# Optimization experiments

Hardware: AMD Instinct MI355X
Metric: run time of the kernel (lower is better)

Reference implementation:

```python
import jax, jax.numpy as jnp
import numpy as np

N_NODES = 50000
N_EDGES = 600000
N_RELS = 16
N_GRAPHS = 128
IN_DIM = 128
REL_LAYERS = [128, 256, 128]
HIDDEN = [128, 256, 128]
N_CLASSES = 8


def setup_inputs() -> dict:
    key = jax.random.key(0)
    ks = jax.random.split(key, 24)
    inp = {}
    inp["h"] = jax.random.normal(ks[0], (N_NODES, IN_DIM), dtype=jnp.float32)
    inp["src"] = jax.random.randint(ks[1], (N_EDGES,), 0, N_NODES)
    inp["dst"] = jax.random.randint(ks[2], (N_EDGES,), 0, N_NODES)
    inp["rel_types"] = jax.random.randint(ks[3], (N_EDGES,), 0, N_RELS)
    inp["graph_ids"] = jnp.sort(jax.random.randint(ks[4], (N_NODES,), 0, N_GRAPHS))
    # RelGraphConv params per layer: W_rel [R,din,dout], W_loop [din,dout], b [dout]
    prev = IN_DIM
    ki = 5
    for i, d in enumerate(REL_LAYERS):
        inp[f"W_rel{i}"] = jax.random.normal(ks[ki], (N_RELS, prev, d), dtype=jnp.float32) * 0.05
        inp[f"W_loop{i}"] = jax.random.normal(ks[ki + 1], (prev, d), dtype=jnp.float32) * 0.05
        inp[f"b{i}"] = jnp.zeros((d,), dtype=jnp.float32)
        prev = d
        ki += 2
    for i, d in enumerate(HIDDEN):
        inp[f"Wh{i}"] = jax.random.normal(ks[ki], (prev, d), dtype=jnp.float32) * 0.05
        inp[f"bh{i}"] = jnp.zeros((d,), dtype=jnp.float32)
        prev = d
        ki += 1
    inp["Wc"] = jax.random.normal(ks[ki], (prev, N_CLASSES), dtype=jnp.float32) * 0.05
    inp["bc"] = jnp.zeros((N_CLASSES,), dtype=jnp.float32)
    return inp


def _rel_graph_conv(h, src, dst, rel, W_rel, W_loop, b):
    # transform every node under every relation: [R, N, dout]
    t = jnp.einsum("nd,rde->rne", h, W_rel)
    msgs = t[rel, src]  # [E, dout] gather per edge
    agg = jax.ops.segment_sum(msgs, dst, num_segments=h.shape[0])
    return jax.nn.relu(agg + h @ W_loop + b)  # self-loop + bias (DGL defaults)


def _forward(h, src, dst, rel_types, graph_ids,
             W_rel0, W_loop0, b0, W_rel1, W_loop1, b1, W_rel2, W_loop2, b2,
             Wh0, bh0, Wh1, bh1, Wh2, bh2, Wc, bc):
    h = h.astype(jnp.float32)
    for Wr, Wl, b in ((W_rel0, W_loop0, b0), (W_rel1, W_loop1, b1), (W_rel2, W_loop2, b2)):
        h = _rel_graph_conv(h, src, dst, rel_types, Wr, Wl, b)
    # dgl.mean_nodes: per-graph mean pooling
    sums = jax.ops.segment_sum(h, graph_ids, num_segments=N_GRAPHS)
    cnts = jax.ops.segment_sum(jnp.ones((h.shape[0],), h.dtype), graph_ids, num_segments=N_GRAPHS)
    hg = sums / jnp.maximum(cnts, 1.0)[:, None]
    for W, b in ((Wh0, bh0), (Wh1, bh1), (Wh2, bh2)):
        hg = jax.nn.relu(hg @ W + b)
    return jax.nn.softmax(hg @ Wc + bc, axis=1)


def reference(h, src, dst, rel_types, graph_ids,
              W_rel0, W_loop0, b0, W_rel1, W_loop1, b1, W_rel2, W_loop2, b2,
              Wh0, bh0, Wh1, bh1, Wh2, bh2, Wc, bc):
    return _forward(h, src, dst, rel_types, graph_ids,
                    W_rel0, W_loop0, b0, W_rel1, W_loop1, b1, W_rel2, W_loop2, b2,
                    Wh0, bh0, Wh1, bh1, Wh2, bh2, Wc, bc)
```

## Files before the change

kernel.cpp:

```cpp
#include <hip/hip_runtime.h>
#include <stdint.h>

#define NN 50000
#define NE 600000
#define NR 16
#define NG 128
#define TS 128
#define SCAN_B 512
#define NB_SCAN ((NN + SCAN_B - 1) / SCAN_B)
#define MAXB 1024

typedef short bf16x8 __attribute__((ext_vector_type(8)));
typedef float f32x4 __attribute__((ext_vector_type(4)));

static __device__ __forceinline__ unsigned short f2bf(float x) {
    unsigned int b = __float_as_uint(x);
    b += 0x7FFFu + ((b >> 16) & 1u);
    return (unsigned short)(b >> 16);
}
static __device__ __forceinline__ float bf2f(unsigned short u) {
    return __uint_as_float(((unsigned int)u) << 16);
}


__global__ void k_hist(const int* __restrict__ rel, const int* __restrict__ dst,
                       const int* __restrict__ src,
                       int* __restrict__ bcnt, int* __restrict__ ncnt,
                       int npc, int nps, int SB, int B) {
    __shared__ int lh[MAXB];
    for (int i = threadIdx.x; i < B; i += 256) lh[i] = 0;
    __syncthreads();
    for (int e = blockIdx.x * blockDim.x + threadIdx.x; e < NE; e += gridDim.x * blockDim.x) {
        int d = dst[e];
        int key = (d / npc) * SB + (src[e] / nps) * NR + rel[e];
        atomicAdd(&lh[key], 1);
        atomicAdd(&ncnt[d], 1);
    }
    __syncthreads();
    for (int i = threadIdx.x; i < B; i += 256) atomicAdd(&bcnt[i], lh[i]);
}

__global__ void k_scan1(const int* __restrict__ ncnt, int* __restrict__ bsum) {
    __shared__ int s[SCAN_B];
    int i = blockIdx.x * SCAN_B + threadIdx.x;
    s[threadIdx.x] = (i < NN) ? ncnt[i] : 0;
    __syncthreads();
    for (int off = SCAN_B / 2; off > 0; off >>= 1) {
        if (threadIdx.x < off) s[threadIdx.x] += s[threadIdx.x + off];
        __syncthreads();
    }
    if (threadIdx.x == 0) bsum[blockIdx.x] = s[0];
}

__global__ void k_scan2(const int* __restrict__ bsum, int* __restrict__ bpref, int* __restrict__ rowptr) {
    if (threadIdx.x == 0 && blockIdx.x == 0) {
        int run = 0;
        for (int b = 0; b < NB_SCAN; ++b) { bpref[b] = run; run += bsum[b]; }
        rowptr[NN] = run;
    }
}

__global__ void k_scan3(const int* __restrict__ ncnt, const int* __restrict__ bpref,
                        int* __restrict__ rowptr) {
    __shared__ int s[SCAN_B];
    int i = blockIdx.x * SCAN_B + threadIdx.x;
    int val = (i < NN) ? ncnt[i] : 0;
    s[threadIdx.x] = val;
    __syncthreads();
    for (int off = 1; off < SCAN_B; off <<= 1) {
        int x = (threadIdx.x >= off) ? s[threadIdx.x - off] : 0;
        __syncthreads();
        s[threadIdx.x] += x;
        __syncthreads();
    }
    if (i < NN) rowptr[i] = bpref[blockIdx.x] + s[threadIdx.x] - val;
}

__global__ __launch_bounds__(1024)
void k_scan_buckets(const int* __restrict__ bcnt, int B, int npc, int SB,
                    const int* __restrict__ rowptr,
                    int* __restrict__ boff, int* __restrict__ tstart,
                    int4* __restrict__ tilemap) {
    __shared__ int s1[MAXB], s2[MAXB];
    __shared__ int e_ex[MAXB + 1], t_ex[MAXB + 1];
    int tid = threadIdx.x;
    int v1 = (tid < B) ? bcnt[tid] : 0;
    int v2 = (v1 + TS - 1) / TS;
    s1[tid] = v1; s2[tid] = v2;
    __syncthreads();
    for (int off = 1; off < MAXB; off <<= 1) {
        int a1 = (tid >= off) ? s1[tid - off] : 0;
        int a2 = (tid >= off) ? s2[tid - off] : 0;
        __syncthreads();
        s1[tid] += a1; s2[tid] += a2;
        __syncthreads();
    }
    if (tid < B) {
        e_ex[tid] = s1[tid] - v1;
        t_ex[tid] = s2[tid] - v2;
        boff[tid] = e_ex[tid];
        tstart[tid] = t_ex[tid];
        if (tid == B - 1) {
            e_ex[B] = s1[tid]; t_ex[B] = s2[tid];
            boff[B] = s1[tid]; tstart[B] = s2[tid];
        }
    }
    __syncthreads();
    int T = t_ex[B];
    for (int t = tid; t < T; t += 1024) {
        int lo = 0, hi = B - 1;
        while (lo < hi) {
            int mid = (lo + hi + 1) >> 1;
            if (t_ex[mid] <= t) lo = mid; else hi = mid - 1;
        }
        int b = lo;
        int tt = t - t_ex[b];
        int v1b = e_ex[b + 1] - e_ex[b];
        int rem = v1b - tt * TS;
        int cnt = rem < TS ? rem : TS;
        int chunk = b / SB;
        int nstart = chunk * npc; if (nstart > NN) nstart = NN;
        tilemap[t] = make_int4(b & (NR - 1), e_ex[b] + tt * TS, cnt, rowptr[nstart]);
    }
}

__global__ void k_scatter(const int* __restrict__ rel, const int* __restrict__ dst,
                          const int* __restrict__ src,
                          const int* __restrict__ boff, int* __restrict__ cursor,
                          const int* __restrict__ rowptr, int* __restrict__ ncur,
                          int* __restrict__ srcs, int* __restrict__ dpos,
                          int npc, int nps, int SB, int B) {
    __shared__ int lh[MAXB];
    const int CH = 4096;
    int e0 = blockIdx.x * CH;
    for (int i = threadIdx.x; i < B; i += 256) lh[i] = 0;
    __syncthreads();
    for (int i = threadIdx.x; i < CH; i += 256) {
        int e = e0 + i;
        if (e < NE) atomicAdd(&lh[(dst[e] / npc) * SB + (src[e] / nps) * NR + rel[e]], 1);
    }
    __syncthreads();
    for (int i = threadIdx.x; i < B; i += 256) {
        int c = lh[i];
        lh[i] = (c > 0) ? atomicAdd(&cursor[i], c) : 0;
    }
    __syncthreads();
    for (int i = threadIdx.x; i < CH; i += 256) {
        int e = e0 + i;
        if (e < NE) {
            int d = dst[e];
            int s = src[e];
            int b = (d / npc) * SB + (s / nps) * NR + rel[e];
            int p = boff[b] + atomicAdd(&lh[b], 1);
            int pd = rowptr[d] + atomicAdd(&ncur[d], 1);
            srcs[p] = s;
            dpos[p] = pd;
        }
    }
}


__global__ void k_hconv(const float* __restrict__ h, unsigned short* __restrict__ hb, int n4) {
    int i = blockIdx.x * 256 + threadIdx.x;
    if (i < n4) {
        float4 v = reinterpret_cast<const float4*>(h)[i];
        ushort4 o = { f2bf(v.x), f2bf(v.y), f2bf(v.z), f2bf(v.w) };
        reinterpret_cast<ushort4*>(hb)[i] = o;
    }
}

__global__ void k_wconv_all(const float* Wr0, const float* Wr1, const float* Wr2,
                            const float* Wl0, const float* Wl1, const float* Wl2,
                            unsigned short* Wt0, unsigned short* Wt1, unsigned short* Wt2,
                            unsigned short* Wlt0, unsigned short* Wlt1, unsigned short* Wlt2) {
    const float* W; unsigned short* O; int R, Kd, Nd;
    switch (blockIdx.y) {
        case 0:  W = Wr0; O = Wt0;  R = NR; Kd = 128; Nd = 128; break;
        case 1:  W = Wr1; O = Wt1;  R = NR; Kd = 128; Nd = 256; break;
        case 2:  W = Wr2; O = Wt2;  R = NR; Kd = 256; Nd = 128; break;
        case 3:  W = Wl0; O = Wlt0; R = 1;  Kd = 128; Nd = 128; break;
        case 4:  W = Wl1; O = Wlt1; R = 1;  Kd = 128; Nd = 256; break;
        default: W = Wl2; O = Wlt2; R = 1;  Kd = 256; Nd = 128; break;
    }
    int total = R * Kd * Nd;
    for (int i = blockIdx.x * 256 + threadIdx.x; i < total; i += gridDim.x * 256) {
        int r = i / (Kd * Nd);
        int rem = i - r * Kd * Nd;
        int k = rem / Nd;
        int n = rem - k * Nd;
        O[((size_t)r * Nd + n) * Kd + k] = f2bf(W[i]);
    }
}


template<int K>
__global__ __launch_bounds__(256, 4)
void k_dense_mfma(const unsigned short* __restrict__ hb,
                  const unsigned short* __restrict__ Wlt,
                  const float* __restrict__ bias,
                  float* __restrict__ outbuf, int ldn) {
    __shared__ __align__(16) unsigned short As[128][72];
    __shared__ __align__(16) unsigned short Bs[128][72];
    const int tid = threadIdx.x;
    const int row0 = blockIdx.x * 128;
    const int colbase = blockIdx.y * 128;
    const int lane = tid & 63, w = tid >> 6;
    const int quad = lane >> 4, col = lane & 15;
    const int srow = tid >> 3, sk = (tid & 7) * 8;

    f32x4 acc[8][2];
#pragma unroll
    for (int i = 0; i < 8; ++i) { acc[i][0] = 0.f; acc[i][1] = 0.f; }

    for (int k0 = 0; k0 < K; k0 += 64) {
        __syncthreads();
#pragma unroll
        for (int pp = 0; pp < 4; ++pp) {
            int rw = pp * 32 + srow;
            int ar = row0 + rw; if (ar >= NN) ar = NN - 1;
            *reinterpret_cast<uint4*>(&As[rw][sk]) =
                *reinterpret_cast<const uint4*>(hb + (size_t)ar * K + k0 + sk);
            *reinterpret_cast<uint4*>(&Bs[rw][sk]) =
                *reinterpret_cast<const uint4*>(Wlt + (size_t)(colbase + rw) * K + k0 + sk);
        }
        __syncthreads();
#pragma unroll
        for (int s = 0; s < 2; ++s) {
            bf16x8 bf0 = *reinterpret_cast<const bf16x8*>(&Bs[w * 32 + col][s * 32 + quad * 8]);
            bf16x8 bf1 = *reinterpret_cast<const bf16x8*>(&Bs[w * 32 + 16 + col][s * 32 + quad * 8]);
#pragma unroll
            for (int rt = 0; rt < 8; ++rt) {
                bf16x8 af = *reinterpret_cast<const bf16x8*>(&As[rt * 16 + col][s * 32 + quad * 8]);
                acc[rt][0] = __builtin_amdgcn_mfma_f32_16x16x32_bf16(af, bf0, acc[rt][0], 0, 0, 0);
                acc[rt][1] = __builtin_amdgcn_mfma_f32_16x16x32_bf16(af, bf1, acc[rt][1], 0, 0, 0);
            }
        }
    }
    float bv0 = bias[colbase + w * 32 + col];
    float bv1 = bias[colbase + w * 32 + 16 + col];
#pragma unroll
    for (int rt = 0; rt < 8; ++rt) {
#pragma unroll
        for (int reg = 0; reg < 4; ++reg) {
            int r = row0 + rt * 16 + quad * 4 + reg;
            if (r < NN) {
                float* dp = outbuf + (size_t)r * ldn + colbase + w * 32;
                dp[col] = acc[rt][0][reg] + bv0;
                dp[16 + col] = acc[rt][1][reg] + bv1;
            }
        }
    }
}


template<int K>
__global__ __launch_bounds__(256, 4)
void k_edge_mfma(const unsigned short* __restrict__ hb,
                 const unsigned short* __restrict__ Wt,
                 int ldn, int colbase,
                 const int* __restrict__ srcs, const int* __restrict__ dpos,
                 const int4* __restrict__ tilemap, const int* __restrict__ tstart,
                 int chunkBase, int SB,
                 unsigned short* __restrict__ msg, int capRows) {
    const int tb0 = tstart[chunkBase];
    const int T = tstart[chunkBase + SB] - tb0;
    const int per = (T + 7) >> 3;
    const int tt = (blockIdx.x & 7) * per + (blockIdx.x >> 3);
    if (tt >= T) return;
    const int4 tm = tilemap[tb0 + tt];
    const int r = tm.x, e0 = tm.y, cnt = tm.z, cES = tm.w;

    __shared__ __align__(16) unsigned short As[128][136];
    __shared__ int s_src[TS], s_out[TS];
    const int tid = threadIdx.x;
    if (tid < TS) {
        int ei = e0 + (tid < cnt ? tid : cnt - 1);
        s_src[tid] = srcs[ei];
        int row = dpos[ei] - cES;
        s_out[tid] = (tid < cnt && row < capRows) ? row : -1;
    }
    __syncthreads();

    const unsigned short* Wb = Wt + ((size_t)r * ldn + colbase) * K;
    const int lane = tid & 63, w = tid >> 6;
    const int quad = lane >> 4, col = lane & 15;
    const int asr = tid >> 4, ask = (tid & 15) * 8;

    f32x4 acc[8][2];
#pragma unroll
    for (int i = 0; i < 8; ++i) { acc[i][0] = 0.f; acc[i][1] = 0.f; }

    for (int kk = 0; kk < K; kk += 128) {
        if (kk) __syncthreads();
#pragma unroll
        for (int q = 0; q < 8; ++q) {
            int rw = q * 16 + asr;
            *reinterpret_cast<uint4*>(&As[rw][ask]) =
                *reinterpret_cast<const uint4*>(hb + (size_t)s_src[rw] * K + kk + ask);
        }
        __syncthreads();
#pragma unroll
        for (int k32 = 0; k32 < 4; ++k32) {
            bf16x8 bf0 = *reinterpret_cast<const bf16x8*>(
                Wb + (size_t)(w * 32 + col) * K + kk + k32 * 32 + quad * 8);
            bf16x8 bf1 = *reinterpret_cast<const bf16x8*>(
                Wb + (size_t)(w * 32 + 16 + col) * K + kk + k32 * 32 + quad * 8);
#pragma unroll
            for (int rt = 0; rt < 8; ++rt) {
                bf16x8 af = *reinterpret_cast<const bf16x8*>(&As[rt * 16 + col][k32 * 32 + quad * 8]);
                acc[rt][0] = __builtin_amdgcn_mfma_f32_16x16x32_bf16(af, bf0, acc[rt][0], 0, 0, 0);
                acc[rt][1] = __builtin_amdgcn_mfma_f32_16x16x32_bf16(af, bf1, acc[rt][1], 0, 0, 0);
            }
        }
    }
#pragma unroll
    for (int rt = 0; rt < 8; ++rt) {
#pragma unroll
        for (int reg = 0; reg < 4; ++reg) {
            int m = rt * 16 + quad * 4 + reg;
            int o = s_out[m];
            if (o >= 0) {
                unsigned short* dp = msg + (size_t)o * 128 + w * 32;
                dp[col] = f2bf(acc[rt][0][reg]);
                dp[16 + col] = f2bf(acc[rt][1][reg]);
            }
        }
    }
}

__global__ __launch_bounds__(256)
void k_reduce(const unsigned short* __restrict__ msg,
              const float* __restrict__ selfb, int ld_self, int co_self,
              unsigned short* __restrict__ out_bf, int ld_bf, int co_bf,
              float* __restrict__ out_f32, int ld_f32, int co_f32,
              const int* __restrict__ rowptr, int n0, int npc, int capRows) {
    int idx = blockIdx.x * 4 + (threadIdx.x >> 6);
    int n = n0 + idx;
    if (idx >= npc || n >= NN) return;
    int lane = threadIdx.x & 63;
    int cES = rowptr[n0];
    float2 acc = *reinterpret_cast<const float2*>(selfb + (size_t)n * ld_self + co_self + lane * 2);
    int j0 = rowptr[n], j1 = rowptr[n + 1];
    int jcap = cES + capRows; if (j1 > jcap) j1 = jcap;
    const unsigned int* mp = reinterpret_cast<const unsigned int*>(msg) + lane;
    int j = j0;
    for (; j + 4 <= j1; j += 4) {
        unsigned int m0 = mp[(size_t)(j + 0 - cES) * 64];
        unsigned int m1 = mp[(size_t)(j + 1 - cES) * 64];
        unsigned int m2 = mp[(size_t)(j + 2 - cES) * 64];
        unsigned int m3 = mp[(size_t)(j + 3 - cES) * 64];
        acc.x += bf2f((unsigned short)(m0 & 0xffffu)) + bf2f((unsigned short)(m1 & 0xffffu))
               + bf2f((unsigned short)(m2 & 0xffffu)) + bf2f((unsigned short)(m3 & 0xffffu));
        acc.y += bf2f((unsigned short)(m0 >> 16)) + bf2f((unsigned short)(m1 >> 16))
               + bf2f((unsigned short)(m2 >> 16)) + bf2f((unsigned short)(m3 >> 16));
    }
    for (; j < j1; ++j) {
        unsigned int m = mp[(size_t)(j - cES) * 64];
        acc.x += bf2f((unsigned short)(m & 0xffffu));
        acc.y += bf2f((unsigned short)(m >> 16));
    }
    acc.x = acc.x > 0.f ? acc.x : 0.f;
    acc.y = acc.y > 0.f ? acc.y : 0.f;
    if (out_bf) {
        unsigned int o = (unsigned int)f2bf(acc.x) | ((unsigned int)f2bf(acc.y) << 16);
        *reinterpret_cast<unsigned int*>(out_bf + (size_t)n * ld_bf + co_bf + lane * 2) = o;
    }
    if (out_f32) {
        *reinterpret_cast<float2*>(out_f32 + (size_t)n * ld_f32 + co_f32 + lane * 2) = acc;
    }
}


__global__ void k_pool(const float* __restrict__ h, const int* __restrict__ gid,
                       float* __restrict__ hg, float* __restrict__ gcnt) {
    const int c = threadIdx.x;
    int n0 = blockIdx.x * 64;
    if (n0 >= NN) return;
    int end = n0 + 64; if (end > NN) end = NN;
    int cur = gid[n0];
    float run = 0.f, crun = 0.f;
    for (int n = n0; n < end; ++n) {
        int g = gid[n];
        if (g != cur) {
            atomicAdd(&hg[cur * 128 + c], run);
            if (c == 0) atomicAdd(&gcnt[cur], crun);
            run = 0.f; crun = 0.f; cur = g;
        }
        run += h[(size_t)n * 128 + c];
        crun += 1.f;
    }
    atomicAdd(&hg[cur * 128 + c], run);
    if (c == 0) atomicAdd(&gcnt[cur], crun);
}

__global__ __launch_bounds__(256)
void k_head(const float* __restrict__ hg, const float* __restrict__ gcnt,
            const float* __restrict__ Wh0, const float* __restrict__ bh0,
            const float* __restrict__ Wh1, const float* __restrict__ bh1,
            const float* __restrict__ Wh2, const float* __restrict__ bh2,
            const float* __restrict__ Wc, const float* __restrict__ bc,
            float* __restrict__ out) {
    __shared__ float x0[128], x1[128], x2[256], x3[128], sl[8];
    int g = blockIdx.x, t = threadIdx.x;
    if (t < 128) {
        float c = gcnt[g];
        x0[t] = hg[g * 128 + t] / (c > 1.f ? c : 1.f);
    }
    __syncthreads();
    if (t < 128) {
        float a = bh0[t];
        for (int k = 0; k < 128; ++k) a += x0[k] * Wh0[k * 128 + t];
        x1[t] = a > 0.f ? a : 0.f;
    }
    __syncthreads();
    {
        float a = bh1[t];
        for (int k = 0; k < 128; ++k) a += x1[k] * Wh1[k * 256 + t];
        x2[t] = a > 0.f ? a : 0.f;
    }
    __syncthreads();
    if (t < 128) {
        float a = bh2[t];
        for (int k = 0; k < 256; ++k) a += x2[k] * Wh2[k * 128 + t];
        x3[t] = a > 0.f ? a : 0.f;
    }
    __syncthreads();
    if (t < 8) {
        float a = bc[t];
        for (int k = 0; k < 128; ++k) a += x3[k] * Wc[k * 8 + t];
        sl[t] = a;
    }
    __syncthreads();
    if (t == 0) {
        float m = sl[0];
        for (int c = 1; c < 8; ++c) m = sl[c] > m ? sl[c] : m;
        float s = 0.f, e[8];
        for (int c = 0; c < 8; ++c) { e[c] = expf(sl[c] - m); s += e[c]; }
        for (int c = 0; c < 8; ++c) out[g * 8 + c] = e[c] / s;
    }
}


extern "C" void kernel_launch(void* const* d_in, const int* in_sizes, int n_in,
                              void* d_out, int out_size, void* d_ws, size_t ws_size,
                              hipStream_t stream) {
    const float* h0   = (const float*)d_in[0];
    const int* src    = (const int*)d_in[1];
    const int* dst    = (const int*)d_in[2];
    const int* rel    = (const int*)d_in[3];
    const int* gid    = (const int*)d_in[4];
    const float* Wr0  = (const float*)d_in[5];
    const float* Wl0  = (const float*)d_in[6];
    const float* b0   = (const float*)d_in[7];
    const float* Wr1  = (const float*)d_in[8];
    const float* Wl1  = (const float*)d_in[9];
    const float* b1   = (const float*)d_in[10];
    const float* Wr2  = (const float*)d_in[11];
    const float* Wl2  = (const float*)d_in[12];
    const float* b2   = (const float*)d_in[13];
    const float* Wh0  = (const float*)d_in[14];
    const float* bh0  = (const float*)d_in[15];
    const float* Wh1  = (const float*)d_in[16];
    const float* bh1  = (const float*)d_in[17];
    const float* Wh2  = (const float*)d_in[18];
    const float* bh2  = (const float*)d_in[19];
    const float* Wc   = (const float*)d_in[20];
    const float* bc   = (const float*)d_in[21];
    float* out = (float*)d_out;

    char* p = (char*)d_ws;
    auto alloc = [&](size_t bytes) { char* q = p; p += (bytes + 255) & ~(size_t)255; return q; };
    float* bufS  = (float*)alloc((size_t)NN * 256 * 4);
    unsigned short* hbA = (unsigned short*)alloc((size_t)NN * 256 * 2);
    unsigned short* hbB = (unsigned short*)alloc((size_t)NN * 128 * 2);
    unsigned short* Wt0 = (unsigned short*)alloc((size_t)NR * 128 * 128 * 2);
    unsigned short* Wt1 = (unsigned short*)alloc((size_t)NR * 256 * 128 * 2);
    unsigned short* Wt2 = (unsigned short*)alloc((size_t)NR * 128 * 256 * 2);
    unsigned short* Wlt0 = (unsigned short*)alloc((size_t)128 * 128 * 2);
    unsigned short* Wlt1 = (unsigned short*)alloc((size_t)256 * 128 * 2);
    unsigned short* Wlt2 = (unsigned short*)alloc((size_t)128 * 256 * 2);
    int* srcs    = (int*)alloc((size_t)NE * 4);
    int* dpos    = (int*)alloc((size_t)NE * 4);
    int* rowptr  = (int*)alloc((size_t)(NN + 1) * 4);
    int* bsum    = (int*)alloc(NB_SCAN * 4);
    int* bpref   = (int*)alloc(NB_SCAN * 4);
    int* boff    = (int*)alloc((MAXB + 1) * 4);
    int* tstart  = (int*)alloc((MAXB + 1) * 4);
    int4* tilemap = (int4*)alloc((size_t)(NE / TS + MAXB + 64) * 16);
    char* zbase  = p;
    int* bcnt    = (int*)alloc(MAXB * 4);
    int* cursor  = (int*)alloc(MAXB * 4);
    int* ncnt    = (int*)alloc((size_t)NN * 4);
    int* ncur    = (int*)alloc((size_t)NN * 4);
    float* hg    = (float*)alloc((size_t)NG * 128 * 4);
    float* gcnt  = (float*)alloc(NG * 4);
    size_t zlen  = (size_t)(p - zbase);
    unsigned short* msg = (unsigned short*)p;

    long long avail = (long long)ws_size - (long long)(p - (char*)d_ws);
    if (avail < (1 << 20)) avail = (1 << 20);
    long long capR64 = avail / 256;
    int C = 64;
    for (int c = 1; c <= 64; ++c) {
        double need = (double)NE / c * 1.15 + 4096.0;
        if ((double)capR64 >= need) { C = c; break; }
    }
    int npc = (NN + C - 1) / C;
    int S = MAXB / (C * NR); if (S < 1) S = 1;
    int SB = S * NR;
    int B = C * SB;
    int nps = (NN + S - 1) / S;
    int capRows = capR64 > 2000000000LL ? 2000000000 : (int)capR64;
    int TPC = (int)((double)NE / C * 1.15 / TS) + SB + 16;
    int RDB = (npc + 3) / 4;

    hipMemsetAsync(zbase, 0, zlen, stream);
    k_hist<<<256, 256, 0, stream>>>(rel, dst, src, bcnt, ncnt, npc, nps, SB, B);
    k_scan1<<<NB_SCAN, SCAN_B, 0, stream>>>(ncnt, bsum);
    k_scan2<<<1, 64, 0, stream>>>(bsum, bpref, rowptr);
    k_scan3<<<NB_SCAN, SCAN_B, 0, stream>>>(ncnt, bpref, rowptr);
    k_scan_buckets<<<1, MAXB, 0, stream>>>(bcnt, B, npc, SB, rowptr, boff, tstart, tilemap);
    k_scatter<<<(NE + 4095) / 4096, 256, 0, stream>>>(rel, dst, src, boff, cursor, rowptr, ncur, srcs, dpos, npc, nps, SB, B);

    k_hconv<<<(NN * 128 / 4 + 255) / 256, 256, 0, stream>>>(h0, hbA, NN * 128 / 4);
    k_wconv_all<<<dim3(512, 6), 256, 0, stream>>>(Wr0, Wr1, Wr2, Wl0, Wl1, Wl2,
                                                  Wt0, Wt1, Wt2, Wlt0, Wlt1, Wlt2);

    const int RB = (NN + TS - 1) / TS;

    k_dense_mfma<128><<<dim3(RB, 1), 256, 0, stream>>>(hbA, Wlt0, b0, bufS, 128);
    for (int c = 0; c < C; ++c) {
        k_edge_mfma<128><<<TPC, 256, 0, stream>>>(hbA, Wt0, 128, 0, srcs, dpos, tilemap, tstart, c * SB, SB, msg, capRows);
        k_reduce<<<RDB, 256, 0, stream>>>(msg, bufS, 128, 0, hbB, 128, 0, (float*)nullptr, 0, 0, rowptr, c * npc, npc, capRows);
    }

    k_dense_mfma<128><<<dim3(RB, 2), 256, 0, stream>>>(hbB, Wlt1, b1, bufS, 256);
    for (int half = 0; half < 2; ++half) {
        for (int c = 0; c < C; ++c) {
            k_edge_mfma<128><<<TPC, 256, 0, stream>>>(hbB, Wt1, 256, half * 128, srcs, dpos, tilemap, tstart, c * SB, SB, msg, capRows);
            k_reduce<<<RDB, 256, 0, stream>>>(msg, bufS, 256, half * 128, hbA, 256, half * 128, (float*)nullptr, 0, 0, rowptr, c * npc, npc, capRows);
        }
    }

    k_dense_mfma<256><<<dim3(RB, 1), 256, 0, stream>>>(hbA, Wlt2, b2, bufS, 128);
    for (int c = 0; c < C; ++c) {
        k_edge_mfma<256><<<TPC, 256, 0, stream>>>(hbA, Wt2, 128, 0, srcs, dpos, tilemap, tstart, c * SB, SB, msg, capRows);
        k_reduce<<<RDB, 256, 0, stream>>>(msg, bufS, 128, 0, (unsigned short*)nullptr, 0, 0, bufS, 128, 0, rowptr, c * npc, npc, capRows);
    }

    k_pool<<<(NN + 63) / 64, 128, 0, stream>>>(bufS, gid, hg, gcnt);
    k_head<<<NG, 256, 0, stream>>>(hg, gcnt, Wh0, bh0, Wh1, bh1, Wh2, bh2, Wc, bc, out);
}
```

Before: 752.7 us.

## Fuse layer-1 column halves into single paired edge and reduce launches

When the workspace fits all edges in one chunk, layer 1's two 128-column halves are computed by one edge-MFMA launch with doubled grid, writing a 256-wide message buffer, and reduced by one 2D-grid reduce launch. This removes a second pass of gathers and launches and lets paired blocks share gathered source rows in cache. It also replaces the strided tile-to-block interleave with a linear mapping for all edge launches. The fused path needs twice the message buffer memory and only activates if the workspace is large enough.

```diff
diff --git a/kernel.cpp b/kernel.cpp
--- a/kernel.cpp
+++ b/kernel.cpp
@@ -257,17 +257,23 @@
 __global__ __launch_bounds__(256, 4)
 void k_edge_mfma(const unsigned short* __restrict__ hb,
                  const unsigned short* __restrict__ Wt,
-                 int ldn, int colbase,
+                 int ldn, int colbase, int msgw, int paired,
                  const int* __restrict__ srcs, const int* __restrict__ dpos,
                  const int4* __restrict__ tilemap, const int* __restrict__ tstart,
                  int chunkBase, int SB,
                  unsigned short* __restrict__ msg, int capRows) {
     const int tb0 = tstart[chunkBase];
     const int T = tstart[chunkBase + SB] - tb0;
-    const int per = (T + 7) >> 3;
-    const int tt = (blockIdx.x & 7) * per + (blockIdx.x >> 3);
-    if (tt >= T) return;
-    const int4 tm = tilemap[tb0 + tt];
+    int t_lin, cb;
+    if (paired) {
+        t_lin = ((blockIdx.x >> 4) << 3) | (blockIdx.x & 7);
+        cb = ((blockIdx.x >> 3) & 1) * 128;
+    } else {
+        t_lin = blockIdx.x;
+        cb = colbase;
+    }
+    if (t_lin >= T) return;
+    const int4 tm = tilemap[tb0 + t_lin];
     const int r = tm.x, e0 = tm.y, cnt = tm.z, cES = tm.w;
 
     __shared__ __align__(16) unsigned short As[128][136];
@@ -281,7 +287,7 @@
     }
     __syncthreads();
 
-    const unsigned short* Wb = Wt + ((size_t)r * ldn + colbase) * K;
+    const unsigned short* Wb = Wt + ((size_t)r * ldn + cb) * K;
     const int lane = tid & 63, w = tid >> 6;
     const int quad = lane >> 4, col = lane & 15;
     const int asr = tid >> 4, ask = (tid & 15) * 8;
@@ -320,7 +326,7 @@
             int m = rt * 16 + quad * 4 + reg;
             int o = s_out[m];
             if (o >= 0) {
-                unsigned short* dp = msg + (size_t)o * 128 + w * 32;
+                unsigned short* dp = msg + (size_t)o * msgw + cb + w * 32;
                 dp[col] = f2bf(acc[rt][0][reg]);
                 dp[16 + col] = f2bf(acc[rt][1][reg]);
             }
@@ -329,7 +335,7 @@
 }
 
 __global__ __launch_bounds__(256)
-void k_reduce(const unsigned short* __restrict__ msg,
+void k_reduce(const unsigned short* __restrict__ msg, int msgw,
               const float* __restrict__ selfb, int ld_self, int co_self,
               unsigned short* __restrict__ out_bf, int ld_bf, int co_bf,
               float* __restrict__ out_f32, int ld_f32, int co_f32,
@@ -338,24 +344,26 @@
     int n = n0 + idx;
     if (idx >= npc || n >= NN) return;
     int lane = threadIdx.x & 63;
+    int cofs = blockIdx.y * 128;
     int cES = rowptr[n0];
-    float2 acc = *reinterpret_cast<const float2*>(selfb + (size_t)n * ld_self + co_self + lane * 2);
+    float2 acc = *reinterpret_cast<const float2*>(selfb + (size_t)n * ld_self + co_self + cofs + lane * 2);
     int j0 = rowptr[n], j1 = rowptr[n + 1];
     int jcap = cES + capRows; if (j1 > jcap) j1 = jcap;
-    const unsigned int* mp = reinterpret_cast<const unsigned int*>(msg) + lane;
+    const int stride = msgw >> 1;
+    const unsigned int* mp = reinterpret_cast<const unsigned int*>(msg) + (cofs >> 1) + lane;
     int j = j0;
     for (; j + 4 <= j1; j += 4) {
-        unsigned int m0 = mp[(size_t)(j + 0 - cES) * 64];
-        unsigned int m1 = mp[(size_t)(j + 1 - cES) * 64];
-        unsigned int m2 = mp[(size_t)(j + 2 - cES) * 64];
-        unsigned int m3 = mp[(size_t)(j + 3 - cES) * 64];
+        unsigned int m0 = mp[(size_t)(j + 0 - cES) * stride];
+        unsigned int m1 = mp[(size_t)(j + 1 - cES) * stride];
+        unsigned int m2 = mp[(size_t)(j + 2 - cES) * stride];
+        unsigned int m3 = mp[(size_t)(j + 3 - cES) * stride];
         acc.x += bf2f((unsigned short)(m0 & 0xffffu)) + bf2f((unsigned short)(m1 & 0xffffu))
                + bf2f((unsigned short)(m2 & 0xffffu)) + bf2f((unsigned short)(m3 & 0xffffu));
         acc.y += bf2f((unsigned short)(m0 >> 16)) + bf2f((unsigned short)(m1 >> 16))
                + bf2f((unsigned short)(m2 >> 16)) + bf2f((unsigned short)(m3 >> 16));
     }
     for (; j < j1; ++j) {
-        unsigned int m = mp[(size_t)(j - cES) * 64];
+        unsigned int m = mp[(size_t)(j - cES) * stride];
         acc.x += bf2f((unsigned short)(m & 0xffffu));
         acc.y += bf2f((unsigned short)(m >> 16));
     }
@@ -363,10 +371,10 @@
     acc.y = acc.y > 0.f ? acc.y : 0.f;
     if (out_bf) {
         unsigned int o = (unsigned int)f2bf(acc.x) | ((unsigned int)f2bf(acc.y) << 16);
-        *reinterpret_cast<unsigned int*>(out_bf + (size_t)n * ld_bf + co_bf + lane * 2) = o;
+        *reinterpret_cast<unsigned int*>(out_bf + (size_t)n * ld_bf + co_bf + cofs + lane * 2) = o;
     }
     if (out_f32) {
-        *reinterpret_cast<float2*>(out_f32 + (size_t)n * ld_f32 + co_f32 + lane * 2) = acc;
+        *reinterpret_cast<float2*>(out_f32 + (size_t)n * ld_f32 + co_f32 + cofs + lane * 2) = acc;
     }
 }
 
@@ -513,6 +521,8 @@
     int capRows = capR64 > 2000000000LL ? 2000000000 : (int)capR64;
     int TPC = (int)((double)NE / C * 1.15 / TS) + SB + 16;
     int RDB = (npc + 3) / 4;
+    int fused = (C == 1 && (double)avail >= (double)NE * 1.15 * 512.0 + 2097152.0) ? 1 : 0;
+    int capRows256 = (int)(avail / 512);
 
     hipMemsetAsync(zbase, 0, zlen, stream);
     k_hist<<<256, 256, 0, stream>>>(rel, dst, src, bcnt, ncnt, npc, nps, SB, B);
@@ -530,22 +540,27 @@
 
     k_dense_mfma<128><<<dim3(RB, 1), 256, 0, stream>>>(hbA, Wlt0, b0, bufS, 128);
     for (int c = 0; c < C; ++c) {
-        k_edge_mfma<128><<<TPC, 256, 0, stream>>>(hbA, Wt0, 128, 0, srcs, dpos, tilemap, tstart, c * SB, SB, msg, capRows);
-        k_reduce<<<RDB, 256, 0, stream>>>(msg, bufS, 128, 0, hbB, 128, 0, (float*)nullptr, 0, 0, rowptr, c * npc, npc, capRows);
+        k_edge_mfma<128><<<TPC, 256, 0, stream>>>(hbA, Wt0, 128, 0, 128, 0, srcs, dpos, tilemap, tstart, c * SB, SB, msg, capRows);
+        k_reduce<<<dim3(RDB, 1), 256, 0, stream>>>(msg, 128, bufS, 128, 0, hbB, 128, 0, (float*)nullptr, 0, 0, rowptr, c * npc, npc, capRows);
     }
 
     k_dense_mfma<128><<<dim3(RB, 2), 256, 0, stream>>>(hbB, Wlt1, b1, bufS, 256);
-    for (int half = 0; half < 2; ++half) {
-        for (int c = 0; c < C; ++c) {
-            k_edge_mfma<128><<<TPC, 256, 0, stream>>>(hbB, Wt1, 256, half * 128, srcs, dpos, tilemap, tstart, c * SB, SB, msg, capRows);
-            k_reduce<<<RDB, 256, 0, stream>>>(msg, bufS, 256, half * 128, hbA, 256, half * 128, (float*)nullptr, 0, 0, rowptr, c * npc, npc, capRows);
+    if (fused) {
+        k_edge_mfma<128><<<2 * TPC, 256, 0, stream>>>(hbB, Wt1, 256, 0, 256, 1, srcs, dpos, tilemap, tstart, 0, SB, msg, capRows256);
+        k_reduce<<<dim3(RDB, 2), 256, 0, stream>>>(msg, 256, bufS, 256, 0, hbA, 256, 0, (float*)nullptr, 0, 0, rowptr, 0, npc, capRows256);
+    } else {
+        for (int half = 0; half < 2; ++half) {
+            for (int c = 0; c < C; ++c) {
+                k_edge_mfma<128><<<TPC, 256, 0, stream>>>(hbB, Wt1, 256, half * 128, 128, 0, srcs, dpos, tilemap, tstart, c * SB, SB, msg, capRows);
+                k_reduce<<<dim3(RDB, 1), 256, 0, stream>>>(msg, 128, bufS, 256, half * 128, hbA, 256, half * 128, (float*)nullptr, 0, 0, rowptr, c * npc, npc, capRows);
+            }
         }
     }
 
     k_dense_mfma<256><<<dim3(RB, 1), 256, 0, stream>>>(hbA, Wlt2, b2, bufS, 128);
     for (int c = 0; c < C; ++c) {
-        k_edge_mfma<256><<<TPC, 256, 0, stream>>>(hbA, Wt2, 128, 0, srcs, dpos, tilemap, tstart, c * SB, SB, msg, capRows);
-        k_reduce<<<RDB, 256, 0, stream>>>(msg, bufS, 128, 0, (unsigned short*)nullptr, 0, 0, bufS, 128, 0, rowptr, c * npc, npc, capRows);
+        k_edge_mfma<256><<<TPC, 256, 0, stream>>>(hbA, Wt2, 128, 0, 128, 0, srcs, dpos, tilemap, tstart, c * SB, SB, msg, capRows);
+        k_reduce<<<dim3(RDB, 1), 256, 0, stream>>>(msg, 128, bufS, 128, 0, (unsigned short*)nullptr, 0, 0, bufS, 128, 0, rowptr, c * npc, npc, capRows);
     }
 
     k_pool<<<(NN + 63) / 64, 128, 0, stream>>>(bufS, gid, hg, gcnt);
```

New measurement: 751.8 us. No clear change (-0.1%).
